# Optimization experiments

Hardware: AMD Instinct MI355X
Metric: run time of the kernel (lower is better)

Reference implementation:

```python
import jax, jax.numpy as jnp
import numpy as np

D_IN = 3
HID = 256
N_BRANCH = 8
SKIP_IN = (4,)
CSG_TREE = [0, 1, [2, 3], [4, 5, [6, 7]]]
FLAG_CONVEX = True
BETA = 100.0
N_POINTS = 100000

# layer dims: [3, 256*7, 8]; layer whose OUTPUT feeds a skip layer emits 256-3=253
_DIMS = [D_IN] + [HID] * 7 + [N_BRANCH]


def _layer_out_dim(layer):
    if (layer + 1) in SKIP_IN:
        return _DIMS[layer + 1] - D_IN
    return _DIMS[layer + 1]


def setup_inputs() -> dict:
    key = jax.random.key(0)
    keys = jax.random.split(key, 20)
    inp = {"x": jax.random.normal(keys[0], (N_POINTS, D_IN), dtype=jnp.float32)}
    n_layers = len(_DIMS) - 1  # 8 linear layers
    for layer in range(n_layers):
        in_d = _DIMS[layer]
        out_d = _layer_out_dim(layer)
        kw = jax.random.fold_in(keys[1], layer)
        if layer == n_layers - 1:  # geometric init of last layer
            W = (np.sqrt(np.pi) / np.sqrt(in_d)
                 + 1e-5 * jax.random.normal(kw, (in_d, out_d), dtype=jnp.float32))
            b = -1.0 * jnp.ones((out_d,), dtype=jnp.float32)
        else:
            W = (np.sqrt(2.0) / np.sqrt(out_d)) * jax.random.normal(
                kw, (in_d, out_d), dtype=jnp.float32)
            b = jnp.zeros((out_d,), dtype=jnp.float32)
        inp[f"W{layer}"] = W
        inp[f"b{layer}"] = b
    return inp


def _softplus_beta(x):
    return jax.nn.softplus(BETA * x) / BETA


def _csg_combine(vals, ops, cvx_flag):
    # hard CSG tree: one-hot matmul == column gather; recursion is static (trace time)
    idxs = [v for v in ops if not isinstance(v, list)]
    cols = [vals[:, jnp.array(idxs)]]
    for v in ops:
        if isinstance(v, list):
            cols.append(_csg_combine(vals, v, not cvx_flag))
    m = jnp.concatenate(cols, axis=1)
    red = jnp.max if cvx_flag else jnp.min
    return red(m, axis=1, keepdims=True)


def _forward(x, Ws, bs):
    inp = x
    h = x
    n_layers = len(Ws)
    inv_sqrt2 = np.float32(1.0 / np.sqrt(2.0))
    for layer in range(n_layers):
        if layer in SKIP_IN:
            h = jnp.concatenate([h, inp], axis=-1) * inv_sqrt2
        h = h @ Ws[layer] + bs[layer]
        if layer < n_layers - 1:
            h = _softplus_beta(h)
    branch_vals = h  # [N, n_branch]
    hcsg = _csg_combine(branch_vals, CSG_TREE, FLAG_CONVEX)  # [N, 1]
    return jnp.concatenate([hcsg, branch_vals], axis=1)  # flag_output == 0


def reference(x, W0, b0, W1, b1, W2, b2, W3, b3, W4, b4, W5, b5, W6, b6, W7, b7):
    Ws = [W0, W1, W2, W3, W4, W5, W6, W7]
    bs = [b0, b1, b2, b3, b4, b5, b6, b7]
    return _forward(x, Ws, bs)
```

## Files before the change

kernel.cpp:

```cpp
#include <hip/hip_runtime.h>
#include <hip/hip_bf16.h>


using bf16x8 = __attribute__((ext_vector_type(8))) __bf16;
using f32x4  = __attribute__((ext_vector_type(4))) float;

#define LDA 264

#define OFFW0 0
#define OFFW1 8192
#define OFFW7 401408
#define WSB_BYTE_OFF 811008
#define OFFB7 1792

#define SCALE_T2 144.26950408889634f
#define INV_SQRT2 0.70710678118654752f
#define LN2_100 0.0069314718055994531f

__device__ __forceinline__ float fast_exp2(float x) {
#if __has_builtin(__builtin_amdgcn_exp2f)
    return __builtin_amdgcn_exp2f(x);
#else
    return exp2f(x);
#endif
}
__device__ __forceinline__ float fast_log2(float x) {
#if __has_builtin(__builtin_amdgcn_logf)
    return __builtin_amdgcn_logf(x);
#else
    return log2f(x);
#endif
}

__device__ __forceinline__ float softplus_t2(float t2) {
    float e = fast_exp2(-fabsf(t2));
    float l = fast_log2(1.0f + e);
    return fmaxf(t2, 0.0f) + l;
}

__device__ __forceinline__ unsigned short bf16_rne(float f) {
    unsigned int u = __float_as_uint(f);
    unsigned int r = u + 0x7FFFu + ((u >> 16) & 1u);
    return (unsigned short)(r >> 16);
}

template <int KK, int MODE, int NT>
__device__ __forceinline__ void layer_mm(
    const unsigned short* __restrict__ wfrag,
    const float* __restrict__ bias,
    unsigned short* act, const float* xst,
    int wave, int lane)
{
    const int quad = lane >> 4;
    const int l15  = lane & 15;

    f32x4 acc[2][NT];
#pragma unroll
    for (int i = 0; i < 2; ++i) {
        const int chb = (wave * 2 + i) * 16 + quad * 4;
        const float4 b4 = *(const float4*)(bias + chb);
#pragma unroll
        for (int nt = 0; nt < NT; ++nt)
            acc[i][nt] = f32x4{b4.x, b4.y, b4.z, b4.w};
    }

    const unsigned short* wbase = wfrag + (wave * 2 * KK * 64 + lane) * 8;

#pragma unroll
    for (int kk = 0; kk < KK; ++kk) {
        bf16x8 bfr[NT];
#pragma unroll
        for (int nt = 0; nt < NT; ++nt)
            bfr[nt] = *(const bf16x8*)(act + (nt * 16 + l15) * LDA + kk * 32 + quad * 8);
#pragma unroll
        for (int i = 0; i < 2; ++i) {
            bf16x8 afr = *(const bf16x8*)(wbase + (i * KK + kk) * 512);
#pragma unroll
            for (int nt = 0; nt < NT; ++nt)
                acc[i][nt] = __builtin_amdgcn_mfma_f32_16x16x32_bf16(afr, bfr[nt], acc[i][nt], 0, 0, 0);
        }
    }

    __syncthreads();

#pragma unroll
    for (int i = 0; i < 2; ++i) {
        const int chb = (wave * 2 + i) * 16 + quad * 4;
#pragma unroll
        for (int nt = 0; nt < NT; ++nt) {
            const int pt = nt * 16 + l15;
            float vv[4];
#pragma unroll
            for (int r = 0; r < 4; ++r) {
                float s = softplus_t2(acc[i][nt][r]);
                if (MODE == 1) {
                    const int ch = chb + r;
                    if (ch >= 253)
                        s = xst[pt * 4 + (ch - 253)];
                }
                vv[r] = s;
            }
            __hip_bfloat162 p01 = __float22bfloat162_rn(float2{vv[0], vv[1]});
            __hip_bfloat162 p23 = __float22bfloat162_rn(float2{vv[2], vv[3]});
            uint2 pk;
            pk.x = *(unsigned int*)&p01;
            pk.y = *(unsigned int*)&p23;
            *(uint2*)(act + pt * LDA + chb) = pk;
        }
    }

    __syncthreads();
}

template <int NT>
__device__ __forceinline__ void run_net(
    const float* __restrict__ x, float* __restrict__ out,
    const unsigned short* __restrict__ wsW, const float* __restrict__ wsB,
    unsigned short* act, float* xst,
    int base_pt, int npts, int tid)
{
    const int wave = tid >> 6, lane = tid & 63;
    const int quad = lane >> 4, l15 = lane & 15;

    for (int i = tid; i < NT * 16 * 32; i += 512) {
        const int pt = i >> 5, ch = i & 31;
        const int ptg = base_pt + pt;
        float v = 0.0f;
        if (ch < 3 && ptg < npts) v = x[ptg * 3 + ch];
        act[pt * LDA + ch] = bf16_rne(v);
        if (ch < 4) xst[pt * 4 + ch] = (ch < 3) ? v : 0.0f;
    }
    __syncthreads();

    layer_mm<1, 0, NT>(wsW + OFFW0, wsB + 0 * 256, act, xst, wave, lane);
    layer_mm<8, 0, NT>(wsW + OFFW1 + 0 * 65536, wsB + 1 * 256, act, xst, wave, lane);
    layer_mm<8, 0, NT>(wsW + OFFW1 + 1 * 65536, wsB + 2 * 256, act, xst, wave, lane);
    layer_mm<8, 1, NT>(wsW + OFFW1 + 2 * 65536, wsB + 3 * 256, act, xst, wave, lane);
    layer_mm<8, 0, NT>(wsW + OFFW1 + 3 * 65536, wsB + 4 * 256, act, xst, wave, lane);
    layer_mm<8, 0, NT>(wsW + OFFW1 + 4 * 65536, wsB + 5 * 256, act, xst, wave, lane);
    layer_mm<8, 0, NT>(wsW + OFFW1 + 5 * 65536, wsB + 6 * 256, act, xst, wave, lane);

    if (wave < NT) {
        const float4 b4 = *(const float4*)(wsB + OFFB7 + quad * 4);
        f32x4 acc = f32x4{b4.x, b4.y, b4.z, b4.w};
        const unsigned short* w7 = wsW + OFFW7;
#pragma unroll
        for (int kk = 0; kk < 8; ++kk) {
            bf16x8 bfr = *(const bf16x8*)(act + (wave * 16 + l15) * LDA + kk * 32 + quad * 8);
            bf16x8 afr = *(const bf16x8*)(w7 + (kk * 64 + lane) * 8);
            acc = __builtin_amdgcn_mfma_f32_16x16x32_bf16(afr, bfr, acc, 0, 0, 0);
        }
        float u0 = __shfl(acc[0], l15 + 16);
        float u1 = __shfl(acc[1], l15 + 16);
        float u2 = __shfl(acc[2], l15 + 16);
        float u3 = __shfl(acc[3], l15 + 16);
        if (quad == 0) {
            const int ptg = base_pt + wave * 16 + l15;
            if (ptg < npts) {
                const float v0 = acc[0], v1 = acc[1], v2 = acc[2], v3 = acc[3];
                const float v4 = u0, v5 = u1, v6 = u2, v7 = u3;
                const float m23   = fminf(v2, v3);
                const float m67   = fmaxf(v6, v7);
                const float m4567 = fminf(fminf(v4, v5), m67);
                const float h     = fmaxf(fmaxf(v0, v1), fmaxf(m23, m4567));
                float* o = out + (long)ptg * 9;
                o[0] = h;
                o[1] = v0; o[2] = v1; o[3] = v2; o[4] = v3;
                o[5] = v4; o[6] = v5; o[7] = v6; o[8] = v7;
            }
        }
    }
}

__global__ __launch_bounds__(512, 4)
void nhrep_main(const float* __restrict__ x, float* __restrict__ out,
                const unsigned short* __restrict__ wsW,
                const float* __restrict__ wsB, int npts, int nbig)
{
    __shared__ unsigned short act[96 * LDA];
    __shared__ float xst[96 * 4];
    const int b = blockIdx.x;
    if (b < nbig) {
        run_net<6>(x, out, wsW, wsB, act, xst, b * 96, npts, threadIdx.x);
    } else {
        run_net<2>(x, out, wsW, wsB, act, xst,
                   nbig * 96 + (b - nbig) * 32, npts, threadIdx.x);
    }
}

struct PackArgs {
    const float* W[8];
    const float* b[8];
};

#define TOTAL_FRAGS 50688
#define TOTAL_BIAS  1808

__global__ void prepack_all(PackArgs args, unsigned short* __restrict__ dstW,
                            float* __restrict__ dstB)
{
    const int t = blockIdx.x * blockDim.x + threadIdx.x;
    const int FB[9]  = {0, 1024, 9216, 17408, 25600, 33792, 41984, 50176, 50688};
    const int KKs[8] = {1, 8, 8, 8, 8, 8, 8, 8};
    const int ind[8] = {3, 256, 256, 256, 256, 256, 256, 256};
    const int outd[8]= {256, 256, 256, 253, 256, 256, 256, 8};

    if (t < TOTAL_FRAGS) {
        int l = 0;
        while (t >= FB[l + 1]) ++l;
        const int f    = t - FB[l];
        const int lane = f & 63;
        const int kk   = (f >> 6) % KKs[l];
        const int mt   = f / (64 * KKs[l]);
        const int o    = mt * 16 + (lane & 15);
        const int kb   = kk * 32 + (lane >> 4) * 8;
        const float* W = args.W[l];
        const int in_d = ind[l], out_d = outd[l];

        unsigned short v[8];
#pragma unroll
        for (int j = 0; j < 8; ++j) {
            const int k = kb + j;
            float w = 0.0f;
            if (k < in_d && o < out_d) {
                float sc = 1.0f;
                if (l == 0) sc = SCALE_T2;
                else if (l == 4) sc = (k < 253) ? INV_SQRT2 : (SCALE_T2 * INV_SQRT2);
                else if (l == 7) sc = LN2_100;
                w = W[k * out_d + o] * sc;
            }
            unsigned int u = __float_as_uint(w);
            v[j] = (unsigned short)((u + 0x7FFFu + ((u >> 16) & 1u)) >> 16);
        }
        uint4 p;
        p.x = (unsigned int)v[0] | ((unsigned int)v[1] << 16);
        p.y = (unsigned int)v[2] | ((unsigned int)v[3] << 16);
        p.z = (unsigned int)v[4] | ((unsigned int)v[5] << 16);
        p.w = (unsigned int)v[6] | ((unsigned int)v[7] << 16);
        *(uint4*)(dstW + (long)t * 8) = p;
    } else if (t < TOTAL_FRAGS + TOTAL_BIAS) {
        const int u = t - TOTAL_FRAGS;
        const int l = (u < 1792) ? (u >> 8) : 7;
        const int idx = (l < 7) ? (u & 255) : (u - 1792);
        const float sc = (l < 7) ? SCALE_T2 : 1.0f;
        dstB[u] = (idx < outd[l]) ? args.b[l][idx] * sc : 0.0f;
    }
}

extern "C" void kernel_launch(void* const* d_in, const int* in_sizes, int n_in,
                              void* d_out, int out_size, void* d_ws, size_t ws_size,
                              hipStream_t stream)
{
    const float* x = (const float*)d_in[0];
    unsigned short* wsW = (unsigned short*)d_ws;
    float* wsB = (float*)((char*)d_ws + WSB_BYTE_OFF);

    PackArgs pa;
    for (int l = 0; l < 8; ++l) {
        pa.W[l] = (const float*)d_in[1 + 2 * l];
        pa.b[l] = (const float*)d_in[2 + 2 * l];
    }
    const int ptot = TOTAL_FRAGS + TOTAL_BIAS;
    prepack_all<<<(ptot + 255) / 256, 256, 0, stream>>>(pa, wsW, wsB);

    const int npts = in_sizes[0] / 3;
    int nbig, nsmall;
    const int tail_pts = 16384;
    if (npts > tail_pts) {
        nbig = (npts - tail_pts + 95) / 96;
        const int base_small = nbig * 96;
        nsmall = (npts - base_small + 31) / 32;
    } else {
        nbig = 0;
        nsmall = (npts + 31) / 32;
    }
    nhrep_main<<<nbig + nsmall, 512, 0, stream>>>(x, (float*)d_out, wsW, wsB,
                                                  npts, nbig);
}
```

Before: 188.6 us.

## Split point tile into two halves and overlap MFMA with softplus epilogue

Each block's points are split into two groups A and B. The matmul of one group is interleaved with the softplus/bf16 epilogue of the other, so matrix-core work overlaps transcendental VALU work, and there is one barrier per half-layer instead of two per layer. The skip-connection splice moves to the epilogue of the matching layer for each group. The cost is doubled accumulator register pressure and reloading each weight fragment twice per layer.

Result: slower. 194.9 us (+3.3%).

```diff
diff --git a/kernel.cpp b/kernel.cpp
--- a/kernel.cpp
+++ b/kernel.cpp
@@ -44,23 +44,22 @@
     return (unsigned short)(r >> 16);
 }
 
-template <int KK, int MODE, int NT>
-__device__ __forceinline__ void layer_mm(
+template <int KK, int NTG>
+__device__ __forceinline__ void mfma_group(
     const unsigned short* __restrict__ wfrag,
     const float* __restrict__ bias,
-    unsigned short* act, const float* xst,
-    int wave, int lane)
+    const unsigned short* act,
+    f32x4 (&acc)[2][NTG], int wave, int lane)
 {
     const int quad = lane >> 4;
     const int l15  = lane & 15;
 
-    f32x4 acc[2][NT];
 #pragma unroll
     for (int i = 0; i < 2; ++i) {
         const int chb = (wave * 2 + i) * 16 + quad * 4;
         const float4 b4 = *(const float4*)(bias + chb);
 #pragma unroll
-        for (int nt = 0; nt < NT; ++nt)
+        for (int nt = 0; nt < NTG; ++nt)
             acc[i][nt] = f32x4{b4.x, b4.y, b4.z, b4.w};
     }
 
@@ -68,37 +67,42 @@
 
 #pragma unroll
     for (int kk = 0; kk < KK; ++kk) {
-        bf16x8 bfr[NT];
-#pragma unroll
-        for (int nt = 0; nt < NT; ++nt)
+        bf16x8 bfr[NTG];
+#pragma unroll
+        for (int nt = 0; nt < NTG; ++nt)
             bfr[nt] = *(const bf16x8*)(act + (nt * 16 + l15) * LDA + kk * 32 + quad * 8);
 #pragma unroll
         for (int i = 0; i < 2; ++i) {
             bf16x8 afr = *(const bf16x8*)(wbase + (i * KK + kk) * 512);
 #pragma unroll
-            for (int nt = 0; nt < NT; ++nt)
+            for (int nt = 0; nt < NTG; ++nt)
                 acc[i][nt] = __builtin_amdgcn_mfma_f32_16x16x32_bf16(afr, bfr[nt], acc[i][nt], 0, 0, 0);
         }
     }
-
-    __syncthreads();
+}
+
+template <int NTG>
+__device__ __forceinline__ void epi_group(
+    f32x4 (&acc)[2][NTG], unsigned short* act, const float* xst,
+    int wave, int lane, bool splice)
+{
+    const int quad = lane >> 4;
+    const int l15  = lane & 15;
 
 #pragma unroll
     for (int i = 0; i < 2; ++i) {
         const int chb = (wave * 2 + i) * 16 + quad * 4;
 #pragma unroll
-        for (int nt = 0; nt < NT; ++nt) {
+        for (int nt = 0; nt < NTG; ++nt) {
             const int pt = nt * 16 + l15;
             float vv[4];
 #pragma unroll
-            for (int r = 0; r < 4; ++r) {
-                float s = softplus_t2(acc[i][nt][r]);
-                if (MODE == 1) {
-                    const int ch = chb + r;
-                    if (ch >= 253)
-                        s = xst[pt * 4 + (ch - 253)];
-                }
-                vv[r] = s;
+            for (int r = 0; r < 4; ++r)
+                vv[r] = softplus_t2(acc[i][nt][r]);
+            if (splice && chb == 252) {
+                vv[1] = xst[pt * 4 + 0];
+                vv[2] = xst[pt * 4 + 1];
+                vv[3] = xst[pt * 4 + 2];
             }
             __hip_bfloat162 p01 = __float22bfloat162_rn(float2{vv[0], vv[1]});
             __hip_bfloat162 p23 = __float22bfloat162_rn(float2{vv[2], vv[3]});
@@ -108,11 +112,9 @@
             *(uint2*)(act + pt * LDA + chb) = pk;
         }
     }
-
-    __syncthreads();
-}
-
-template <int NT>
+}
+
+template <int NTG>
 __device__ __forceinline__ void run_net(
     const float* __restrict__ x, float* __restrict__ out,
     const unsigned short* __restrict__ wsW, const float* __restrict__ wsB,
@@ -122,7 +124,7 @@
     const int wave = tid >> 6, lane = tid & 63;
     const int quad = lane >> 4, l15 = lane & 15;
 
-    for (int i = tid; i < NT * 16 * 32; i += 512) {
+    for (int i = tid; i < 2 * NTG * 16 * 32; i += 512) {
         const int pt = i >> 5, ch = i & 31;
         const int ptg = base_pt + pt;
         float v = 0.0f;
@@ -132,15 +134,38 @@
     }
     __syncthreads();
 
-    layer_mm<1, 0, NT>(wsW + OFFW0, wsB + 0 * 256, act, xst, wave, lane);
-    layer_mm<8, 0, NT>(wsW + OFFW1 + 0 * 65536, wsB + 1 * 256, act, xst, wave, lane);
-    layer_mm<8, 0, NT>(wsW + OFFW1 + 1 * 65536, wsB + 2 * 256, act, xst, wave, lane);
-    layer_mm<8, 1, NT>(wsW + OFFW1 + 2 * 65536, wsB + 3 * 256, act, xst, wave, lane);
-    layer_mm<8, 0, NT>(wsW + OFFW1 + 3 * 65536, wsB + 4 * 256, act, xst, wave, lane);
-    layer_mm<8, 0, NT>(wsW + OFFW1 + 4 * 65536, wsB + 5 * 256, act, xst, wave, lane);
-    layer_mm<8, 0, NT>(wsW + OFFW1 + 5 * 65536, wsB + 6 * 256, act, xst, wave, lane);
-
-    if (wave < NT) {
+    unsigned short* actA = act;
+    unsigned short* actB = act + NTG * 16 * LDA;
+    const float* xstA = xst;
+    const float* xstB = xst + NTG * 16 * 4;
+
+    f32x4 accA[2][NTG], accB[2][NTG];
+
+    mfma_group<1, NTG>(wsW + OFFW0, wsB, actA, accA, wave, lane);
+    __syncthreads();
+
+    mfma_group<1, NTG>(wsW + OFFW0, wsB, actB, accB, wave, lane);
+    epi_group<NTG>(accA, actA, xstA, wave, lane, false);
+    __syncthreads();
+
+#pragma unroll 1
+    for (int l = 1; l <= 6; ++l) {
+        const unsigned short* Wl = wsW + OFFW1 + (l - 1) * 65536;
+        const float* bl = wsB + l * 256;
+
+        mfma_group<8, NTG>(Wl, bl, actA, accA, wave, lane);
+        epi_group<NTG>(accB, actB, xstB, wave, lane, l == 4);
+        __syncthreads();
+
+        mfma_group<8, NTG>(Wl, bl, actB, accB, wave, lane);
+        epi_group<NTG>(accA, actA, xstA, wave, lane, l == 3);
+        __syncthreads();
+    }
+
+    epi_group<NTG>(accB, actB, xstB, wave, lane, false);
+    __syncthreads();
+
+    if (wave < 2 * NTG) {
         const float4 b4 = *(const float4*)(wsB + OFFB7 + quad * 4);
         f32x4 acc = f32x4{b4.x, b4.y, b4.z, b4.w};
         const unsigned short* w7 = wsW + OFFW7;
@@ -181,9 +206,9 @@
     __shared__ float xst[96 * 4];
     const int b = blockIdx.x;
     if (b < nbig) {
-        run_net<6>(x, out, wsW, wsB, act, xst, b * 96, npts, threadIdx.x);
+        run_net<3>(x, out, wsW, wsB, act, xst, b * 96, npts, threadIdx.x);
     } else {
-        run_net<2>(x, out, wsW, wsB, act, xst,
+        run_net<1>(x, out, wsW, wsB, act, xst,
                    nbig * 96 + (b - nbig) * 32, npts, threadIdx.x);
     }
 }
```
